# Kernel tuning notes

Hardware: AMD Instinct MI355X
Metric: run time of the kernel (lower is better)

Reference implementation:

```python
import jax, jax.numpy as jnp
import numpy as np

E = 1024      # embed_dim
H = 16        # num_heads
HD = E // H   # head_dim = 64
M = 64        # num_landmarks


def setup_inputs() -> dict:
    key = jax.random.key(0)
    ks = jax.random.split(key, 9)
    B, Lq, Lk = 2, 2048, 2048
    inv = 1.0 / np.sqrt(E)
    return {
        "query": jax.random.normal(ks[0], (B, Lq, E), dtype=jnp.float32),
        "key":   jax.random.normal(ks[1], (B, Lk, E), dtype=jnp.float32),
        "value": jax.random.normal(ks[2], (B, Lk, E), dtype=jnp.float32),
        # learned params (xavier-ish scale)
        "Wv": jax.random.normal(ks[3], (E, E), dtype=jnp.float32) * inv,
        "bv": jnp.zeros((E,), dtype=jnp.float32),
        "Wl": jax.random.normal(ks[4], (M, E), dtype=jnp.float32) * inv,
        "bl": jnp.zeros((M,), dtype=jnp.float32),
        "Wo": jax.random.normal(ks[5], (E, E), dtype=jnp.float32) * inv,
        "bo": jnp.zeros((E,), dtype=jnp.float32),
    }


def reference(query, key, value, Wv, bv, Wl, bl, Wo, bo):
    B, Lq, _ = query.shape
    Lk = key.shape[1]
    # value projection -> [B, H, Lk, HD]
    v = (value @ Wv.T + bv).reshape(B, Lk, H, HD).transpose(0, 2, 1, 3)
    # landmark projections + softmax over landmark dim
    ql = jax.nn.softmax((query @ Wl.T + bl) / np.sqrt(M), axis=-1)  # [B, Lq, M]
    kl = jax.nn.softmax((key @ Wl.T + bl) / np.sqrt(M), axis=-1)    # [B, Lk, M]
    # landmark attention: [B, Lq, Lk], scaled by sqrt(head_dim), softmax over keys
    attn = jax.nn.softmax(
        jnp.einsum("bqm,bkm->bqk", ql, kl) / np.sqrt(HD), axis=-1)
    # apply shared attention across heads: [B, H, Lq, HD]
    out_h = jnp.einsum("bqk,bhkd->bhqd", attn, v)
    out = out_h.transpose(0, 2, 1, 3).reshape(B, Lq, E)
    return out @ Wo.T + bo
```

## Files before the change

kernel.cpp:

```cpp
#include <hip/hip_runtime.h>
#include <hip/hip_bf16.h>
#include <cstdint>

typedef unsigned short u16;
typedef __attribute__((ext_vector_type(8))) short short8;
typedef __attribute__((ext_vector_type(4))) float f32x4;
typedef __attribute__((ext_vector_type(4))) unsigned short us4;

__device__ __forceinline__ u16 f2bf(float f) {
    union { float f; unsigned int i; } v; v.f = f;
    unsigned int x = v.i;
    unsigned int r = x + 0x7fffu + ((x >> 16) & 1u);
    return (u16)(r >> 16);
}

enum { EPI_F32 = 0, EPI_BF16 = 1, EPI_EXP_RS = 3, EPI_F32_DIV_CB = 4, EPI_LMSM = 5 };

template <int BM, int BN, int EPI, bool AF32, bool BF32>
__device__ __forceinline__ void gemm_body(
    char* __restrict__ smem,
    const void* __restrict__ Ax, const void* __restrict__ A2x,
    const void* __restrict__ Bx, void* __restrict__ Cv,
    int M, int N, int K, long sA, long sB, long sC,
    const float* __restrict__ biasCol, float* __restrict__ rowScale, float expScale,
    int m0, int n0, int z)
{
    constexpr int BK = 64;
    constexpr int MFRAG = (BM + 31) / 32;
    constexpr int NFRAG = BN / 32;
    constexpr int AG = (BM + 31) / 32;
    constexpr int BG = BN / 32;
    u16* As = (u16*)smem;
    u16* Bs = (u16*)(smem + (long)BM * BK * 2);

    const int tid = threadIdx.x;
    const int lane = tid & 63;
    const int quad = lane >> 4;
    const int l15 = lane & 15;
    const int w = tid >> 6;
    const int wm = w >> 1, wn = w & 1;

    const int r8 = tid >> 3;
    const int cl = tid & 7;
    const int cg = ((cl ^ (r8 & 7)) * 8);

    const u16* ap[AG];
    const float* apf[AG];
    if constexpr (AF32) {
        const float* base = (const float*)Ax;
        long mr = m0;
        if (A2x != nullptr && m0 >= (M >> 1)) { base = (const float*)A2x; mr = m0 - (M >> 1); }
        const float* Afb = base + (long)z * sA + (long)mr * K;
#pragma unroll
        for (int j = 0; j < AG; ++j) apf[j] = Afb + (long)(j * 32 + r8) * K + cg;
    } else {
        const u16* Ab = (const u16*)Ax + (long)z * sA + (long)m0 * K;
#pragma unroll
        for (int j = 0; j < AG; ++j) ap[j] = Ab + (long)(j * 32 + r8) * K + cg;
    }
    const u16* bp[BG];
    const float* bpf[BG];
    if constexpr (BF32) {
        const float* Bfb = (const float*)Bx + (long)z * sB + (long)n0 * K;
#pragma unroll
        for (int j = 0; j < BG; ++j) bpf[j] = Bfb + (long)(j * 32 + r8) * K + cg;
    } else {
        const u16* Bb = (const u16*)Bx + (long)z * sB + (long)n0 * K;
#pragma unroll
        for (int j = 0; j < BG; ++j) bp[j] = Bb + (long)(j * 32 + r8) * K + cg;
    }

    f32x4 acc[MFRAG][NFRAG] = {};

    const int sw = l15 & 7;

    for (int k0 = 0; k0 < K; k0 += BK) {
        if constexpr (!AF32) {
#pragma unroll
            for (int j = 0; j < AG; ++j) {
                __builtin_amdgcn_global_load_lds(
                    (const __attribute__((address_space(1))) void*)(ap[j]),
                    (__attribute__((address_space(3))) void*)(&As[(j * 32 + r8) * BK + cl * 8]),
                    16, 0, 0);
                ap[j] += BK;
            }
        }
        if constexpr (!BF32) {
#pragma unroll
            for (int j = 0; j < BG; ++j) {
                __builtin_amdgcn_global_load_lds(
                    (const __attribute__((address_space(1))) void*)(bp[j]),
                    (__attribute__((address_space(3))) void*)(&Bs[(j * 32 + r8) * BK + cl * 8]),
                    16, 0, 0);
                bp[j] += BK;
            }
        }
        if constexpr (AF32) {
#pragma unroll
            for (int j = 0; j < AG; ++j) {
                const float4 u0 = *(const float4*)(apf[j]);
                const float4 u1 = *(const float4*)(apf[j] + 4);
                short8 o;
                o[0] = (short)f2bf(u0.x); o[1] = (short)f2bf(u0.y);
                o[2] = (short)f2bf(u0.z); o[3] = (short)f2bf(u0.w);
                o[4] = (short)f2bf(u1.x); o[5] = (short)f2bf(u1.y);
                o[6] = (short)f2bf(u1.z); o[7] = (short)f2bf(u1.w);
                *(short8*)&As[(j * 32 + r8) * BK + cl * 8] = o;
                apf[j] += BK;
            }
        }
        if constexpr (BF32) {
#pragma unroll
            for (int j = 0; j < BG; ++j) {
                const float4 u0 = *(const float4*)(bpf[j]);
                const float4 u1 = *(const float4*)(bpf[j] + 4);
                short8 o;
                o[0] = (short)f2bf(u0.x); o[1] = (short)f2bf(u0.y);
                o[2] = (short)f2bf(u0.z); o[3] = (short)f2bf(u0.w);
                o[4] = (short)f2bf(u1.x); o[5] = (short)f2bf(u1.y);
                o[6] = (short)f2bf(u1.z); o[7] = (short)f2bf(u1.w);
                *(short8*)&Bs[(j * 32 + r8) * BK + cl * 8] = o;
                bpf[j] += BK;
            }
        }
        __syncthreads();
#pragma unroll
        for (int ks = 0; ks < 2; ++ks) {
            short8 af[MFRAG], bfr[NFRAG];
#pragma unroll
            for (int i = 0; i < MFRAG; ++i)
                af[i] = *(const short8*)&As[(wm * (BM / 2) + i * 16 + l15) * BK +
                                            (((ks * 4 + quad) ^ sw) * 8)];
#pragma unroll
            for (int i = 0; i < NFRAG; ++i)
                bfr[i] = *(const short8*)&Bs[(wn * (BN / 2) + i * 16 + l15) * BK +
                                             (((ks * 4 + quad) ^ sw) * 8)];
#pragma unroll
            for (int i = 0; i < MFRAG; ++i)
#pragma unroll
                for (int jn = 0; jn < NFRAG; ++jn)
                    acc[i][jn] = __builtin_amdgcn_mfma_f32_16x16x32_bf16(af[i], bfr[jn], acc[i][jn], 0, 0, 0);
        }
        __syncthreads();
    }

    if constexpr (EPI == EPI_LMSM) {
        float* red = (float*)(smem + (long)(BM + BN) * BK * 2);
        float ev[4][NFRAG];
#pragma unroll
        for (int r = 0; r < 4; ++r) {
            float s = 0.f;
#pragma unroll
            for (int jn = 0; jn < NFRAG; ++jn) {
                const int col = wn * (BN / 2) + jn * 16 + l15;
                float v = exp2f((acc[0][jn][r] + biasCol[col]) * expScale);
                ev[r][jn] = v; s += v;
            }
            s += __shfl_xor(s, 1); s += __shfl_xor(s, 2);
            s += __shfl_xor(s, 4); s += __shfl_xor(s, 8);
            if (l15 == 0) red[wn * BM + wm * 16 + quad * 4 + r] = s;
        }
        __syncthreads();
#pragma unroll
        for (int r = 0; r < 4; ++r) {
            const int mrow = wm * 16 + quad * 4 + r;
            const float inv = 1.0f / (red[mrow] + red[BM + mrow]);
            const long m = m0 + mrow;
#pragma unroll
            for (int jn = 0; jn < NFRAG; ++jn) {
                const int col = wn * (BN / 2) + jn * 16 + l15;
                ((u16*)Cv)[m * N + col] = f2bf(ev[r][jn] * inv);
            }
        }
        return;
    } else {
#pragma unroll
        for (int i = 0; i < MFRAG; ++i) {
            const int mb = m0 + wm * (BM / 2) + i * 16 + quad * 4;
#pragma unroll
            for (int r = 0; r < 4; ++r) {
                const int m = mb + r;
                float rin = 0.f;
                if constexpr (EPI == EPI_F32_DIV_CB) rin = 1.0f / rowScale[(long)z * M + m];
                float rowsum = 0.f;
#pragma unroll
                for (int jn = 0; jn < NFRAG; ++jn) {
                    const int col = n0 + wn * (BN / 2) + jn * 16 + l15;
                    float v = acc[i][jn][r];
                    if constexpr (EPI == EPI_EXP_RS) { v = exp2f(v * expScale); rowsum += v; }
                    if constexpr (EPI == EPI_F32_DIV_CB) v = v * rin + biasCol[col];
                    if constexpr (EPI == EPI_F32 || EPI == EPI_F32_DIV_CB)
                        ((float*)Cv)[(long)z * sC + (long)m * N + col] = v;
                    else
                        ((u16*)Cv)[(long)z * sC + (long)m * N + col] = f2bf(v);
                }
                if constexpr (EPI == EPI_EXP_RS) {
                    rowsum += __shfl_xor(rowsum, 1);
                    rowsum += __shfl_xor(rowsum, 2);
                    rowsum += __shfl_xor(rowsum, 4);
                    rowsum += __shfl_xor(rowsum, 8);
                    if (l15 == 0) atomicAdd(&rowScale[(long)z * M + m], rowsum);
                }
            }
        }
    }
}

template <int BM, int BN, int EPI, bool AF32, bool BF32>
__global__ void __launch_bounds__(256)
gemm_bt(const void* __restrict__ Ax, const void* __restrict__ A2x,
        const void* __restrict__ Bx, void* __restrict__ Cv,
        int M, int N, int K, long sA, long sB, long sC,
        const float* __restrict__ biasCol, float* __restrict__ rowScale, float expScale)
{
    extern __shared__ char smem[];
    gemm_body<BM, BN, EPI, AF32, BF32>(smem, Ax, A2x, Bx, Cv, M, N, K, sA, sB, sC,
                                       biasCol, rowScale, expScale,
                                       blockIdx.y * BM, blockIdx.x * BN, blockIdx.z);
}

__global__ void __launch_bounds__(256)
fused23(const float* __restrict__ query, const float* __restrict__ key,
        const u16* __restrict__ Wlb, u16* __restrict__ qlkl,
        const float* __restrict__ bl,
        const float* __restrict__ Wo, const u16* __restrict__ WvT, u16* __restrict__ Wov)
{
    extern __shared__ char smem[];
    const int b = blockIdx.x;
    if (b < 256) {
        gemm_body<32, 64, EPI_LMSM, true, false>(smem, query, key, Wlb, qlkl,
            8192, 64, 1024, 0, 0, 0, bl, nullptr, 0.18033688011112042f,
            b * 32, 0, 0);
    } else {
        const int t = b - 256;
        gemm_body<64, 64, EPI_BF16, true, false>(smem, Wo, nullptr, WvT, Wov,
            1024, 1024, 1024, 0, 0, 0, nullptr, nullptr, 0.f,
            (t >> 4) * 64, (t & 15) * 64, 0);
    }
}

__global__ void __launch_bounds__(256)
fused45(const u16* __restrict__ Wov, const float* __restrict__ value, u16* __restrict__ Ut,
        const u16* __restrict__ qlkl, u16* __restrict__ Pm, float* __restrict__ rsc)
{
    extern __shared__ char smem[];
    const int b = blockIdx.x;
    if (b < 512) {
        const int x = b & 31, y = (b >> 5) & 7, z = b >> 8;
        gemm_body<128, 64, EPI_BF16, false, true>(smem, Wov, nullptr, value, Ut,
            1024, 2048, 1024, 0, 2097152, 2097152, nullptr, nullptr, 0.f,
            y * 128, x * 64, z);
    } else {
        const int t = b - 512;
        const int x = t & 15, y = (t >> 4) & 15, z = t >> 8;
        gemm_body<128, 128, EPI_EXP_RS, false, false>(smem, qlkl, nullptr, qlkl + 262144, Pm,
            2048, 2048, 64, 131072, 131072, 4194304, nullptr, rsc, 0.18033688011112042f,
            y * 128, x * 128, z);
    }
}

__global__ void __launch_bounds__(256)
prep_all(const float* __restrict__ Wl, const float* __restrict__ Wv,
         const float* __restrict__ Wo, const float* __restrict__ bv,
         const float* __restrict__ bo,
         u16* __restrict__ Wlb, u16* __restrict__ WvT,
         float* __restrict__ rsc, float* __restrict__ bocomb)
{
    __shared__ float t[64][65];
    const int b = blockIdx.x;
    const int tid = threadIdx.x;
    if (b < 64) {
        long i = ((long)b * 256 + tid) * 4;
        const float4 v = *(const float4*)(Wl + i);
        us4 o;
        o.x = f2bf(v.x); o.y = f2bf(v.y); o.z = f2bf(v.z); o.w = f2bf(v.w);
        *(us4*)(Wlb + i) = o;
    } else if (b < 320) {
        const int bidx = b - 64;
        const int bx = bidx & 15, by = bidx >> 4;
#pragma unroll
        for (int p = 0; p < 16; ++p) {
            int idx = p * 256 + tid;
            int r = idx >> 6, c = idx & 63;
            t[r][c] = Wv[(long)(by * 64 + r) * 1024 + bx * 64 + c];
        }
        __syncthreads();
#pragma unroll
        for (int p = 0; p < 16; ++p) {
            int idx = p * 256 + tid;
            int c = idx >> 6, r = idx & 63;
            WvT[(long)(bx * 64 + c) * 1024 + by * 64 + r] = f2bf(t[r][c]);
        }
        if (bx == 0) rsc[by * 256 + tid] = 0.f;
    } else {
        const int row = (b - 320) * 4 + (tid >> 6);
        const int lane = tid & 63;
        float s = 0.f;
#pragma unroll
        for (int i = 0; i < 16; ++i) s += Wo[(long)row * 1024 + i * 64 + lane] * bv[i * 64 + lane];
        for (int o = 32; o; o >>= 1) s += __shfl_xor(s, o, 64);
        if (lane == 0) bocomb[row] = bo[row] + s;
    }
}

extern "C" void kernel_launch(void* const* d_in, const int* in_sizes, int n_in,
                              void* d_out, int out_size, void* d_ws, size_t ws_size,
                              hipStream_t stream)
{
    const float* query = (const float*)d_in[0];
    const float* key   = (const float*)d_in[1];
    const float* value = (const float*)d_in[2];
    const float* Wv    = (const float*)d_in[3];
    const float* bv    = (const float*)d_in[4];
    const float* Wl    = (const float*)d_in[5];
    const float* bl    = (const float*)d_in[6];
    const float* Wo    = (const float*)d_in[7];
    const float* bo    = (const float*)d_in[8];
    float* out = (float*)d_out;

    char* ws = (char*)d_ws;
    u16*   Wlb    = (u16*)  (ws + 25165824);
    u16*   WvT    = (u16*)  (ws + 27394048);
    u16*   Wov    = (u16*)  (ws + 29491200);
    u16*   qlkl   = (u16*)  (ws + 31588352);
    u16*   Ut     = (u16*)  (ws + 32636928);
    u16*   Pm     = (u16*)  (ws + 41025536);
    float* rsc    = (float*)(ws + 57802752);
    float* bocomb = (float*)(ws + 57819136);

    prep_all<<<dim3(576), 256, 0, stream>>>(Wl, Wv, Wo, bv, bo,
                                            Wlb, WvT, rsc, bocomb);

    fused23<<<dim3(512), 256, 16384, stream>>>(query, key, Wlb, qlkl, bl,
                                               Wo, WvT, Wov);

    fused45<<<dim3(1024), 256, 32768, stream>>>(Wov, value, Ut, qlkl, Pm, rsc);

    gemm_bt<64, 128, EPI_F32_DIV_CB, false, false>
        <<<dim3(8, 32, 2), 256, 24576, stream>>>(
        Pm, nullptr, Ut, out, 2048, 1024, 2048,
        4194304, 2097152, 2097152, bocomb, rsc, 0.f);
}
```

Baseline: 178.0 us.

## Split K across two wave groups in final attention-output GEMM

Replaces the generic final GEMM (P·Ut with row-normalize and bias) with a dedicated kernel using 512 threads, where two 256-thread halves each process half of the K=2048 reduction, then combine partial accumulators through shared memory before the epilogue. This doubles the waves per block to improve latency hiding and occupancy for a grid of only 512 blocks. It costs extra LDS (48KB), a shared-memory reduction step, and the loop uses single-buffered loads with two barriers per iteration.

Measured after the change: 171.0 us. -4.0%, faster.

```diff
diff --git a/kernel.cpp b/kernel.cpp
--- a/kernel.cpp
+++ b/kernel.cpp
@@ -206,19 +206,6 @@
     }
 }
 
-template <int BM, int BN, int EPI, bool AF32, bool BF32>
-__global__ void __launch_bounds__(256)
-gemm_bt(const void* __restrict__ Ax, const void* __restrict__ A2x,
-        const void* __restrict__ Bx, void* __restrict__ Cv,
-        int M, int N, int K, long sA, long sB, long sC,
-        const float* __restrict__ biasCol, float* __restrict__ rowScale, float expScale)
-{
-    extern __shared__ char smem[];
-    gemm_body<BM, BN, EPI, AF32, BF32>(smem, Ax, A2x, Bx, Cv, M, N, K, sA, sB, sC,
-                                       biasCol, rowScale, expScale,
-                                       blockIdx.y * BM, blockIdx.x * BN, blockIdx.z);
-}
-
 __global__ void __launch_bounds__(256)
 fused23(const float* __restrict__ query, const float* __restrict__ key,
         const u16* __restrict__ Wlb, u16* __restrict__ qlkl,
@@ -256,6 +243,112 @@
         gemm_body<128, 128, EPI_EXP_RS, false, false>(smem, qlkl, nullptr, qlkl + 262144, Pm,
             2048, 2048, 64, 131072, 131072, 4194304, nullptr, rsc, 0.18033688011112042f,
             y * 128, x * 128, z);
+    }
+}
+
+__global__ void __launch_bounds__(512)
+gemm6_sk(const u16* __restrict__ Pm, const u16* __restrict__ Ut, float* __restrict__ out,
+         const float* __restrict__ bocomb, const float* __restrict__ rsc)
+{
+    extern __shared__ char smem[];
+    const int tid = threadIdx.x;
+    const int kh = tid >> 8;
+    const int gtid = tid & 255;
+    const int lane = tid & 63;
+    const int quad = lane >> 4;
+    const int l15 = lane & 15;
+    const int w4 = (tid >> 6) & 3;
+    const int wm = w4 >> 1, wn = w4 & 1;
+    const int z = blockIdx.z;
+    const int m0 = blockIdx.y * 64;
+    const int n0 = blockIdx.x * 128;
+
+    u16* As = (u16*)(smem + kh * 24576);
+    u16* Bs = As + 64 * 64;
+
+    const int r8 = gtid >> 3;
+    const int cl = gtid & 7;
+    const int cg = ((cl ^ (r8 & 7)) * 8);
+
+    const u16* Ab = Pm + (long)z * 4194304 + (long)m0 * 2048 + kh * 1024;
+    const u16* Bb = Ut + (long)z * 2097152 + (long)n0 * 2048 + kh * 1024;
+    const u16* ap[2];
+    const u16* bp[4];
+#pragma unroll
+    for (int j = 0; j < 2; ++j) ap[j] = Ab + (long)(j * 32 + r8) * 2048 + cg;
+#pragma unroll
+    for (int j = 0; j < 4; ++j) bp[j] = Bb + (long)(j * 32 + r8) * 2048 + cg;
+
+    f32x4 acc[2][4] = {};
+    const int sw = l15 & 7;
+
+    for (int k0 = 0; k0 < 1024; k0 += 64) {
+#pragma unroll
+        for (int j = 0; j < 2; ++j) {
+            __builtin_amdgcn_global_load_lds(
+                (const __attribute__((address_space(1))) void*)(ap[j]),
+                (__attribute__((address_space(3))) void*)(&As[(j * 32 + r8) * 64 + cl * 8]),
+                16, 0, 0);
+            ap[j] += 64;
+        }
+#pragma unroll
+        for (int j = 0; j < 4; ++j) {
+            __builtin_amdgcn_global_load_lds(
+                (const __attribute__((address_space(1))) void*)(bp[j]),
+                (__attribute__((address_space(3))) void*)(&Bs[(j * 32 + r8) * 64 + cl * 8]),
+                16, 0, 0);
+            bp[j] += 64;
+        }
+        __syncthreads();
+#pragma unroll
+        for (int ks = 0; ks < 2; ++ks) {
+            short8 af[2], bfr[4];
+#pragma unroll
+            for (int i = 0; i < 2; ++i)
+                af[i] = *(const short8*)&As[(wm * 32 + i * 16 + l15) * 64 +
+                                            (((ks * 4 + quad) ^ sw) * 8)];
+#pragma unroll
+            for (int i = 0; i < 4; ++i)
+                bfr[i] = *(const short8*)&Bs[(wn * 64 + i * 16 + l15) * 64 +
+                                             (((ks * 4 + quad) ^ sw) * 8)];
+#pragma unroll
+            for (int i = 0; i < 2; ++i)
+#pragma unroll
+                for (int jn = 0; jn < 4; ++jn)
+                    acc[i][jn] = __builtin_amdgcn_mfma_f32_16x16x32_bf16(af[i], bfr[jn], acc[i][jn], 0, 0, 0);
+        }
+        __syncthreads();
+    }
+
+    if (kh == 1) {
+#pragma unroll
+        for (int i = 0; i < 2; ++i)
+#pragma unroll
+            for (int jn = 0; jn < 4; ++jn)
+                *(f32x4*)(smem + (((i * 4 + jn) * 256 + gtid) << 4)) = acc[i][jn];
+    }
+    __syncthreads();
+    if (kh == 0) {
+#pragma unroll
+        for (int i = 0; i < 2; ++i)
+#pragma unroll
+            for (int jn = 0; jn < 4; ++jn)
+                acc[i][jn] += *(const f32x4*)(smem + (((i * 4 + jn) * 256 + gtid) << 4));
+#pragma unroll
+        for (int i = 0; i < 2; ++i) {
+            const int mb = m0 + wm * 32 + i * 16 + quad * 4;
+#pragma unroll
+            for (int r = 0; r < 4; ++r) {
+                const int m = mb + r;
+                const float rin = 1.0f / rsc[z * 2048 + m];
+#pragma unroll
+                for (int jn = 0; jn < 4; ++jn) {
+                    const int col = n0 + wn * 64 + jn * 16 + l15;
+                    out[(long)z * 2097152 + (long)m * 1024 + col] =
+                        acc[i][jn][r] * rin + bocomb[col];
+                }
+            }
+        }
     }
 }
 
@@ -336,8 +429,5 @@
 
     fused45<<<dim3(1024), 256, 32768, stream>>>(Wov, value, Ut, qlkl, Pm, rsc);
 
-    gemm_bt<64, 128, EPI_F32_DIV_CB, false, false>
-        <<<dim3(8, 32, 2), 256, 24576, stream>>>(
-        Pm, nullptr, Ut, out, 2048, 1024, 2048,
-        4194304, 2097152, 2097152, bocomb, rsc, 0.f);
-}
+    gemm6_sk<<<dim3(8, 32, 2), 512, 49152, stream>>>(Pm, Ut, out, bocomb, rsc);
+}
```

## Double-buffer GEMM LDS tiles to overlap next-tile loads with MFMA compute

Applied to the files above, without the earlier changes.

The shared GEMM body now keeps two LDS tile buffers and prefetches the next K-tile while MFMAs run on the current one. Async global-to-LDS loads go straight into the alternate buffer, and fp32 operands are read into registers early and converted to bf16 after compute. This removes one barrier per iteration and hides global load latency. The cost is doubled LDS per block, which may lower occupancy, plus higher register pressure from the staged fp32 values.

Result: faster. 165.8 us (median of 2 runs) (-6.9%).

```diff
diff --git a/kernel.cpp b/kernel.cpp
--- a/kernel.cpp
+++ b/kernel.cpp
@@ -30,8 +30,7 @@
     constexpr int NFRAG = BN / 32;
     constexpr int AG = (BM + 31) / 32;
     constexpr int BG = BN / 32;
-    u16* As = (u16*)smem;
-    u16* Bs = (u16*)(smem + (long)BM * BK * 2);
+    constexpr int TBUF = (BM + BN) * BK;
 
     const int tid = threadIdx.x;
     const int lane = tid & 63;
@@ -71,10 +70,13 @@
     }
 
     f32x4 acc[MFRAG][NFRAG] = {};
-
     const int sw = l15 & 7;
-
-    for (int k0 = 0; k0 < K; k0 += BK) {
+    u16* const base16 = (u16*)smem;
+    const int NT = K / BK;
+
+    {
+        u16* As = base16;
+        u16* Bs = base16 + BM * BK;
         if constexpr (!AF32) {
 #pragma unroll
             for (int j = 0; j < AG; ++j) {
@@ -84,18 +86,7 @@
                     16, 0, 0);
                 ap[j] += BK;
             }
-        }
-        if constexpr (!BF32) {
-#pragma unroll
-            for (int j = 0; j < BG; ++j) {
-                __builtin_amdgcn_global_load_lds(
-                    (const __attribute__((address_space(1))) void*)(bp[j]),
-                    (__attribute__((address_space(3))) void*)(&Bs[(j * 32 + r8) * BK + cl * 8]),
-                    16, 0, 0);
-                bp[j] += BK;
-            }
-        }
-        if constexpr (AF32) {
+        } else {
 #pragma unroll
             for (int j = 0; j < AG; ++j) {
                 const float4 u0 = *(const float4*)(apf[j]);
@@ -109,7 +100,16 @@
                 apf[j] += BK;
             }
         }
-        if constexpr (BF32) {
+        if constexpr (!BF32) {
+#pragma unroll
+            for (int j = 0; j < BG; ++j) {
+                __builtin_amdgcn_global_load_lds(
+                    (const __attribute__((address_space(1))) void*)(bp[j]),
+                    (__attribute__((address_space(3))) void*)(&Bs[(j * 32 + r8) * BK + cl * 8]),
+                    16, 0, 0);
+                bp[j] += BK;
+            }
+        } else {
 #pragma unroll
             for (int j = 0; j < BG; ++j) {
                 const float4 u0 = *(const float4*)(bpf[j]);
@@ -123,29 +123,102 @@
                 bpf[j] += BK;
             }
         }
-        __syncthreads();
+    }
+    __syncthreads();
+
+    for (int t = 0; t < NT; ++t) {
+        u16* Asc = base16 + (t & 1) * TBUF;
+        u16* Bsc = Asc + BM * BK;
+        u16* Asn = base16 + ((t + 1) & 1) * TBUF;
+        u16* Bsn = Asn + BM * BK;
+        const bool pf = (t + 1 < NT);
+
+        float4 ra[AG][2];
+        float4 rb[BG][2];
+        if (pf) {
+            if constexpr (!AF32) {
+#pragma unroll
+                for (int j = 0; j < AG; ++j) {
+                    __builtin_amdgcn_global_load_lds(
+                        (const __attribute__((address_space(1))) void*)(ap[j]),
+                        (__attribute__((address_space(3))) void*)(&Asn[(j * 32 + r8) * BK + cl * 8]),
+                        16, 0, 0);
+                    ap[j] += BK;
+                }
+            } else {
+#pragma unroll
+                for (int j = 0; j < AG; ++j) {
+                    ra[j][0] = *(const float4*)(apf[j]);
+                    ra[j][1] = *(const float4*)(apf[j] + 4);
+                    apf[j] += BK;
+                }
+            }
+            if constexpr (!BF32) {
+#pragma unroll
+                for (int j = 0; j < BG; ++j) {
+                    __builtin_amdgcn_global_load_lds(
+                        (const __attribute__((address_space(1))) void*)(bp[j]),
+                        (__attribute__((address_space(3))) void*)(&Bsn[(j * 32 + r8) * BK + cl * 8]),
+                        16, 0, 0);
+                    bp[j] += BK;
+                }
+            } else {
+#pragma unroll
+                for (int j = 0; j < BG; ++j) {
+                    rb[j][0] = *(const float4*)(bpf[j]);
+                    rb[j][1] = *(const float4*)(bpf[j] + 4);
+                    bpf[j] += BK;
+                }
+            }
+        }
+
 #pragma unroll
         for (int ks = 0; ks < 2; ++ks) {
             short8 af[MFRAG], bfr[NFRAG];
 #pragma unroll
             for (int i = 0; i < MFRAG; ++i)
-                af[i] = *(const short8*)&As[(wm * (BM / 2) + i * 16 + l15) * BK +
-                                            (((ks * 4 + quad) ^ sw) * 8)];
+                af[i] = *(const short8*)&Asc[(wm * (BM / 2) + i * 16 + l15) * BK +
+                                             (((ks * 4 + quad) ^ sw) * 8)];
 #pragma unroll
             for (int i = 0; i < NFRAG; ++i)
-                bfr[i] = *(const short8*)&Bs[(wn * (BN / 2) + i * 16 + l15) * BK +
-                                             (((ks * 4 + quad) ^ sw) * 8)];
+                bfr[i] = *(const short8*)&Bsc[(wn * (BN / 2) + i * 16 + l15) * BK +
+                                              (((ks * 4 + quad) ^ sw) * 8)];
 #pragma unroll
             for (int i = 0; i < MFRAG; ++i)
 #pragma unroll
                 for (int jn = 0; jn < NFRAG; ++jn)
                     acc[i][jn] = __builtin_amdgcn_mfma_f32_16x16x32_bf16(af[i], bfr[jn], acc[i][jn], 0, 0, 0);
         }
+
+        if (pf) {
+            if constexpr (AF32) {
+#pragma unroll
+                for (int j = 0; j < AG; ++j) {
+                    short8 o;
+                    o[0] = (short)f2bf(ra[j][0].x); o[1] = (short)f2bf(ra[j][0].y);
+                    o[2] = (short)f2bf(ra[j][0].z); o[3] = (short)f2bf(ra[j][0].w);
+                    o[4] = (short)f2bf(ra[j][1].x); o[5] = (short)f2bf(ra[j][1].y);
+                    o[6] = (short)f2bf(ra[j][1].z); o[7] = (short)f2bf(ra[j][1].w);
+                    *(short8*)&Asn[(j * 32 + r8) * BK + cl * 8] = o;
+                }
+            }
+            if constexpr (BF32) {
+#pragma unroll
+                for (int j = 0; j < BG; ++j) {
+                    short8 o;
+                    o[0] = (short)f2bf(rb[j][0].x); o[1] = (short)f2bf(rb[j][0].y);
+                    o[2] = (short)f2bf(rb[j][0].z); o[3] = (short)f2bf(rb[j][0].w);
+                    o[4] = (short)f2bf(rb[j][1].x); o[5] = (short)f2bf(rb[j][1].y);
+                    o[6] = (short)f2bf(rb[j][1].z); o[7] = (short)f2bf(rb[j][1].w);
+                    *(short8*)&Bsn[(j * 32 + r8) * BK + cl * 8] = o;
+                }
+            }
+        }
         __syncthreads();
     }
 
     if constexpr (EPI == EPI_LMSM) {
-        float* red = (float*)(smem + (long)(BM + BN) * BK * 2);
+        float* red = (float*)(base16 + 2 * TBUF);
         float ev[4][NFRAG];
 #pragma unroll
         for (int r = 0; r < 4; ++r) {
@@ -331,13 +404,13 @@
     prep_all<<<dim3(576), 256, 0, stream>>>(Wl, Wv, Wo, bv, bo,
                                             Wlb, WvT, rsc, bocomb);
 
-    fused23<<<dim3(512), 256, 16384, stream>>>(query, key, Wlb, qlkl, bl,
+    fused23<<<dim3(512), 256, 32768, stream>>>(query, key, Wlb, qlkl, bl,
                                                Wo, WvT, Wov);
 
-    fused45<<<dim3(1024), 256, 32768, stream>>>(Wov, value, Ut, qlkl, Pm, rsc);
+    fused45<<<dim3(1024), 256, 49152, stream>>>(Wov, value, Ut, qlkl, Pm, rsc);
 
     gemm_bt<64, 128, EPI_F32_DIV_CB, false, false>
-        <<<dim3(8, 32, 2), 256, 24576, stream>>>(
+        <<<dim3(8, 32, 2), 256, 49152, stream>>>(
         Pm, nullptr, Ut, out, 2048, 1024, 2048,
         4194304, 2097152, 2097152, bocomb, rsc, 0.f);
 }
```
